# Optimization experiments

Hardware: AMD Instinct MI355X
Metric: run time of the kernel (lower is better)

Reference implementation:

```python
import jax, jax.numpy as jnp
import numpy as np

B, S, HID, NH, NKV, HD, PS = 4, 1024, 4096, 32, 8, 128, 16
PPS = S // PS            # pages per sequence
NP = B * PPS             # total pages
NNZ = B * S


def _llama31_freqs(head_dim):
    # flashinfer apply_llama31_rope defaults: theta=5e5, scale=8, low=1, high=4, old_ctx=8192
    half = head_dim // 2
    theta, scale, low_ff, high_ff, old_ctx = 500000.0, 8.0, 1.0, 4.0, 8192.0
    freq = 1.0 / (theta ** (jnp.arange(half, dtype=jnp.float32) * 2.0 / head_dim))
    wavelen = 2.0 * jnp.pi / freq
    low_wl, high_wl = old_ctx / low_ff, old_ctx / high_ff
    smooth = (old_ctx / wavelen - low_ff) / (high_ff - low_ff)
    return jnp.where(wavelen < high_wl, freq,
                     jnp.where(wavelen > low_wl, freq / scale,
                               (1.0 - smooth) * freq / scale + smooth * freq))


def _rope(x, pos, freqs):
    # x: [nnz, H, D], non-interleaved (rotate-half) layout
    ang = pos.astype(jnp.float32)[:, None] * freqs[None, :]          # [nnz, D/2]
    cos, sin = jnp.cos(ang)[:, None, :], jnp.sin(ang)[:, None, :]    # [nnz, 1, D/2]
    x1, x2 = jnp.split(x, 2, axis=-1)
    return jnp.concatenate([x1 * cos - x2 * sin, x2 * cos + x1 * sin], axis=-1)


def setup_inputs() -> dict:
    key = jax.random.key(0)
    ks = jax.random.split(key, 6)
    std = 0.02
    return {
        "hidden_states": jax.random.normal(ks[0], (NNZ, HID), jnp.float32),
        "wq": jax.random.normal(ks[1], (NH * HD, HID), jnp.float32) * std,
        "wk": jax.random.normal(ks[2], (NKV * HD, HID), jnp.float32) * std,
        "wv": jax.random.normal(ks[3], (NKV * HD, HID), jnp.float32) * std,
        "wo": jax.random.normal(ks[4], (HID, NH * HD), jnp.float32) * std,
        "kv_cache": jnp.zeros((1, NP, 2, PS, NKV, HD), jnp.float32),
        "position_ids": jnp.tile(jnp.arange(S, dtype=jnp.int32), B),
        "kv_page_indices": jnp.arange(NP, dtype=jnp.int32),
        "kv_page_indptr": jnp.arange(B + 1, dtype=jnp.int32) * PPS,
        "kv_last_page_lens": jnp.full((B,), PS, jnp.int32),
        "qo_indptr": jnp.arange(B + 1, dtype=jnp.int32) * S,
    }


def reference(hidden_states, wq, wk, wv, wo, kv_cache, position_ids,
              kv_page_indices, kv_page_indptr, kv_last_page_lens, qo_indptr):
    nnz = hidden_states.shape[0]
    b = qo_indptr.shape[0] - 1
    s = nnz // b
    # fused QKV projections (nn.Linear stores [out, in])
    q = (hidden_states @ wq.T).reshape(nnz, NH, HD)
    k = (hidden_states @ wk.T).reshape(nnz, NKV, HD)
    v = (hidden_states @ wv.T).reshape(nnz, NKV, HD)
    # inline Llama-3.1 RoPE with per-token position ids
    freqs = _llama31_freqs(HD)
    q = _rope(q, position_ids, freqs)
    k = _rope(k, position_ids, freqs)
    # paged-KV append: scatter k/v into pages at (page_id, slot)
    cache = kv_cache[0]                                   # [NP, 2, PS, NKV, HD]
    ps = cache.shape[2]
    pages = kv_page_indices.reshape(b, -1)                # [B, PPS]
    bidx = jnp.repeat(jnp.arange(b), s)
    pid = pages[bidx, position_ids // ps]
    slot = position_ids % ps
    cache = cache.at[pid, 0, slot].set(k).at[pid, 1, slot].set(v)
    # paged attention: gather per-sequence K/V from pages, causal SDPA with GQA
    flat = pages.reshape(-1)
    kf = cache[flat, 0].reshape(b, s, NKV, HD)
    vf = cache[flat, 1].reshape(b, s, NKV, HD)
    g = NH // NKV
    kr = jnp.repeat(kf, g, axis=2)                        # [B, S, NH, HD]
    vr = jnp.repeat(vf, g, axis=2)
    qb = q.reshape(b, s, NH, HD)
    scale = 1.0 / jnp.sqrt(jnp.float32(HD))
    scores = jnp.einsum('bqhd,bkhd->bhqk', qb, kr) * scale
    mask = jnp.tril(jnp.ones((s, s), bool))
    scores = jnp.where(mask[None, None], scores, jnp.float32(-1e30))
    attn = jax.nn.softmax(scores, axis=-1)
    out = jnp.einsum('bhqk,bkhd->bqhd', attn, vr).reshape(nnz, NH * HD)
    return out @ wo.T
```

## Files before the change

### kernel.cpp

```cpp
#include <hip/hip_runtime.h>

typedef unsigned short u16;
typedef __bf16 bf16x8 __attribute__((ext_vector_type(8)));
typedef float f32x4 __attribute__((ext_vector_type(4)));

__device__ __forceinline__ u16 f2bf(float f) {
  unsigned int u = __float_as_uint(f);
  u += 0x7fffu + ((u >> 16) & 1u);
  return (u16)(u >> 16);
}
__device__ __forceinline__ float bf2f(u16 v) {
  return __uint_as_float(((unsigned int)v) << 16);
}

__device__ __forceinline__ void gl_lds16(const u16* g, u16* l) {
  auto* lp = reinterpret_cast<__attribute__((address_space(3))) unsigned int*>(
      reinterpret_cast<uintptr_t>(l));
  auto* gp = reinterpret_cast<const __attribute__((address_space(1))) unsigned int*>(
      reinterpret_cast<uintptr_t>(g));
  __builtin_amdgcn_global_load_lds(gp, lp, 16, 0, 0);
}

__global__ __launch_bounds__(256) void cvt_kernel(const float* __restrict__ in,
                                                  u16* __restrict__ out, int n4) {
  int i = blockIdx.x * 256 + threadIdx.x;
  if (i >= n4) return;
  float4 v = ((const float4*)in)[i];
  ushort4 o;
  o.x = f2bf(v.x); o.y = f2bf(v.y); o.z = f2bf(v.z); o.w = f2bf(v.w);
  ((ushort4*)out)[i] = o;
}


#define BARRIER() __builtin_amdgcn_s_barrier()
#define VMCNT(n_) asm volatile("s_waitcnt vmcnt(" #n_ ")" ::: "memory")
#define PH_SYNC()                                           \
  do {                                                      \
    BARRIER();                                              \
    asm volatile("s_waitcnt lgkmcnt(0)" ::: "memory");      \
    __builtin_amdgcn_sched_barrier(0);                      \
  } while (0)

#define STAGE_A(b_, h_, kt_)                                                        \
  gl_lds16(gA + (size_t)((h_) * 128) * K + (size_t)(kt_) * 32,                      \
           lds + (b_) * 16384 + (h_) * 4096 + w * 512)

#define STAGE_B(b_, h_, kt_)                                                        \
  gl_lds16(gB + (size_t)((h_) * 128) * K + (size_t)(kt_) * 32,                      \
           lds + (b_) * 16384 + 8192 + (h_) * 4096 + w * 512)

#define LOADS_A(b_, qm_)                                                            \
  do {                                                                              \
    _Pragma("unroll") for (int i2 = 0; i2 < 4; i2++)                                \
      ar[i2] = *(const bf16x8*)&lds[(b_) * 16384 + arow + ((qm_)*4 + i2) * 512 + ax]; \
  } while (0)

#define LOADS_B(b_, qn_)                                                            \
  do {                                                                              \
    _Pragma("unroll") for (int j2 = 0; j2 < 2; j2++)                                \
      br[(qn_)*2 + j2] =                                                            \
          *(const bf16x8*)&lds[(b_) * 16384 + brow + ((qn_)*2 + j2) * 512 + ax];    \
  } while (0)

#define MFMA_Q(qm_, qn_)                                                            \
  do {                                                                              \
    __builtin_amdgcn_s_setprio(1);                                                  \
    _Pragma("unroll") for (int i2 = 0; i2 < 4; i2++) {                              \
      _Pragma("unroll") for (int j2 = 0; j2 < 2; j2++) {                            \
        acc[(qm_)*4 + i2][(qn_)*2 + j2] = __builtin_amdgcn_mfma_f32_16x16x32_bf16(  \
            ar[i2], br[(qn_)*2 + j2], acc[(qm_)*4 + i2][(qn_)*2 + j2], 0, 0, 0);    \
      }                                                                             \
    }                                                                               \
    __builtin_amdgcn_s_setprio(0);                                                  \
  } while (0)

template <int OUT_BF16>
__global__ __launch_bounds__(512, 2) void gemm8p(const u16* __restrict__ A,
                                                 const u16* __restrict__ B,
                                                 void* __restrict__ Cv,
                                                 int M, int N, int K) {
  __shared__ u16 lds[32768];
  (void)M;
  const int t = threadIdx.x, lane = t & 63, w = t >> 6;
  const int col = lane & 15, quad = lane >> 4;
  const int wm = w >> 2, wn = w & 3;

  const int nwg = gridDim.x * gridDim.y;
  const int wgid = blockIdx.y * gridDim.x + blockIdx.x;
  const int xcd = wgid & 7, lin = wgid >> 3;
  const int q8 = nwg >> 3, r8 = nwg & 7;
  const int nid = (xcd < r8 ? xcd * (q8 + 1) : r8 * (q8 + 1) + (xcd - r8) * q8) + lin;
  const int m0 = (nid / gridDim.x) * 256;
  const int n0 = (nid % gridDim.x) * 256;

  const int pr_ = t >> 3;
  const int s_ = (t & 7) ^ (pr_ & 7);
  const int srow = (pr_ << 1) | (s_ >> 2);
  const int sj = s_ & 3;
  const u16* gA = A + (size_t)(m0 + srow) * K + sj * 8;
  const u16* gB = B + (size_t)(n0 + srow) * K + sj * 8;

  const int arow = wm * 4096;
  const int brow = 8192 + wn * 2048;
  const int ax = (col >> 1) * 64 +
                 (((((col & 1) << 2) | quad) ^ (col >> 1)) << 3);

  f32x4 acc[8][4] = {};
  bf16x8 ar[4], br[4];

  STAGE_A(0, 0, 0); STAGE_A(0, 1, 0);
  STAGE_B(0, 0, 0); STAGE_B(0, 1, 0);
  STAGE_B(1, 0, 1); STAGE_B(1, 1, 1);
  VMCNT(2);
  BARRIER();

  const int NIT = K >> 6;
  for (int it = 0; it < NIT - 1; ++it) {
    const int kt = it * 2;
    LOADS_A(0, 0); LOADS_B(0, 0);
    STAGE_A(1, 0, kt + 1);
    PH_SYNC(); MFMA_Q(0, 0); BARRIER();
    LOADS_B(0, 1);
    STAGE_A(1, 1, kt + 1);
    PH_SYNC(); MFMA_Q(0, 1); BARRIER();
    LOADS_A(0, 1);
    STAGE_B(0, 0, kt + 2);
    PH_SYNC(); MFMA_Q(1, 0); BARRIER();
    STAGE_B(0, 1, kt + 2);
    PH_SYNC(); MFMA_Q(1, 1); VMCNT(2); BARRIER();
    LOADS_A(1, 0); LOADS_B(1, 0);
    STAGE_A(0, 0, kt + 2);
    PH_SYNC(); MFMA_Q(0, 0); BARRIER();
    LOADS_B(1, 1);
    STAGE_A(0, 1, kt + 2);
    PH_SYNC(); MFMA_Q(0, 1); BARRIER();
    LOADS_A(1, 1);
    STAGE_B(1, 0, kt + 3);
    PH_SYNC(); MFMA_Q(1, 0); BARRIER();
    STAGE_B(1, 1, kt + 3);
    PH_SYNC(); MFMA_Q(1, 1); VMCNT(2); BARRIER();
  }

  {
    const int kl = 2 * NIT - 1;
    LOADS_A(0, 0); LOADS_B(0, 0);
    STAGE_A(1, 0, kl);
    PH_SYNC(); MFMA_Q(0, 0); BARRIER();
    LOADS_B(0, 1);
    STAGE_A(1, 1, kl);
    PH_SYNC(); MFMA_Q(0, 1); BARRIER();
    LOADS_A(0, 1);
    PH_SYNC(); MFMA_Q(1, 0); BARRIER();
    PH_SYNC(); MFMA_Q(1, 1); VMCNT(0); BARRIER();
    LOADS_A(1, 0); LOADS_B(1, 0);
    PH_SYNC(); MFMA_Q(0, 0); BARRIER();
    LOADS_B(1, 1);
    PH_SYNC(); MFMA_Q(0, 1); BARRIER();
    LOADS_A(1, 1);
    PH_SYNC(); MFMA_Q(1, 0); BARRIER();
    MFMA_Q(1, 1);
  }

#pragma unroll
  for (int i = 0; i < 8; i++) {
#pragma unroll
    for (int j = 0; j < 4; j++) {
      const int mb = m0 + wm * 128 + i * 16 + quad * 4;
      const int n = n0 + wn * 64 + j * 16 + col;
#pragma unroll
      for (int r = 0; r < 4; r++) {
        float v = acc[i][j][r];
        if constexpr (OUT_BF16)
          ((u16*)Cv)[(size_t)(mb + r) * N + n] = f2bf(v);
        else
          ((float*)Cv)[(size_t)(mb + r) * N + n] = v;
      }
    }
  }
}

__global__ __launch_bounds__(256) void transpose_kernel(const u16* __restrict__ in,
                                                        u16* __restrict__ out,
                                                        int in_stride, int out_stride) {
  __shared__ u16 tile[64][72];
  const int t = threadIdx.x;
  const int bm = blockIdx.y;
  const int bn = blockIdx.x;
  const int r = t >> 3, c = (t & 7) * 8;
  const u16* src = in + (size_t)(bm * 64 + r) * in_stride + bn * 64 + c;
  *(uint4*)&tile[r][c] = *(const uint4*)src;
  *(uint4*)&tile[r + 32][c] = *(const uint4*)(src + (size_t)32 * in_stride);
  __syncthreads();
  u16 vals[8];
  u16* dst = out + (size_t)(bn * 64 + r) * out_stride + bm * 64 + c;
#pragma unroll
  for (int i = 0; i < 8; i++) vals[i] = tile[c + i][r];
  *(uint4*)dst = *(uint4*)vals;
#pragma unroll
  for (int i = 0; i < 8; i++) vals[i] = tile[c + i][r + 32];
  *(uint4*)(dst + (size_t)32 * out_stride) = *(uint4*)vals;
}

__global__ __launch_bounds__(256) void rope_kernel(u16* __restrict__ X,
                                                   const int* __restrict__ pos_ids,
                                                   int log2H, int row_stride) {
  int tid = blockIdx.x * 256 + threadIdx.x;
  int i = tid & 63;
  int rest = tid >> 6;
  int h = rest & ((1 << log2H) - 1);
  int token = rest >> log2H;
  float pos = (float)pos_ids[token];
  float fr = __builtin_exp2f(-(float)i * (18.93156856932417f / 64.0f));
  float wl = 6.283185307179586f / fr;
  float f2;
  if (wl < 2048.0f) f2 = fr;
  else if (wl > 8192.0f) f2 = fr * 0.125f;
  else {
    float sm = (8192.0f / wl - 1.0f) * (1.0f / 3.0f);
    f2 = (1.0f - sm) * fr * 0.125f + sm * fr;
  }
  float ang = pos * f2;
  float ss = sinf(ang), cc = cosf(ang);
  size_t base = (size_t)token * row_stride + (size_t)h * 128 + i;
  float x1 = bf2f(X[base]), x2 = bf2f(X[base + 64]);
  X[base] = f2bf(x1 * cc - x2 * ss);
  X[base + 64] = f2bf(x2 * cc + x1 * ss);
}

__global__ __launch_bounds__(256, 2) void attn_kernel(const u16* __restrict__ Qg,
                                                      const u16* __restrict__ Kg,
                                                      const u16* __restrict__ VTg,
                                                      u16* __restrict__ Og,
                                                      int QS, int KS) {
  const int qtp = 7 - blockIdx.x;
  const int qA = qtp * 2, qB = qA + 1;
  const int h = blockIdx.y, b = blockIdx.z;
  const int kvh = h >> 2;
  const int t = threadIdx.x, lane = t & 63, w = t >> 6;
  const int col = lane & 15, quad = lane >> 4;

  __shared__ u16 Ks[2][64 * 128];
  __shared__ u16 Vt[2][128 * 64];
  __shared__ u16 Ps[4][16][72];

  const u16* Kbase = Kg + (size_t)(b * 1024) * KS + kvh * 128;
  const u16* Vbase = VTg + (size_t)(kvh * 128) * 4096 + b * 1024;

  auto stage_kv = [&](int bb, int j) {
#pragma unroll
    for (int c = 0; c < 4; c++) {
      int ch = w * 4 + c;
      int krow = ch * 4 + (lane >> 4);
      int kg = (lane & 15) ^ (krow & 15);
      gl_lds16(Kbase + (size_t)(j * 64 + krow) * KS + kg * 8, &Ks[bb][ch * 512]);
      int vrow = ch * 8 + (lane >> 3);
      int vg = (lane & 7) ^ (vrow & 7);
      gl_lds16(Vbase + (size_t)vrow * 4096 + j * 64 + vg * 8, &Vt[bb][ch * 512]);
    }
  };

  {
    const u16* QbA = Qg + (size_t)(b * 1024 + qA * 64) * QS + h * 128;
    const u16* QbB = Qg + (size_t)(b * 1024 + qB * 64) * QS + h * 128;
#pragma unroll
    for (int c = 0; c < 4; c++) {
      int ch = w * 4 + c;
      int row = ch * 4 + (lane >> 4);
      int g = (lane & 15) ^ (row & 15);
      gl_lds16(QbA + (size_t)row * QS + g * 8, &Ks[0][ch * 512]);
      gl_lds16(QbB + (size_t)row * QS + g * 8, &Vt[0][ch * 512]);
    }
  }
  stage_kv(1, 0);
  __syncthreads();
  bf16x8 qaA[4], qaB[4];
#pragma unroll
  for (int kk = 0; kk < 4; kk++) {
    int row = w * 16 + col;
    int off = row * 128 + (((quad + 4 * kk) ^ col) << 3);
    qaA[kk] = *(const bf16x8*)&Ks[0][off];
    qaB[kk] = *(const bf16x8*)&Vt[0][off];
  }
  BARRIER();

  f32x4 oA[8] = {}, oB[8] = {};
  float mA[4] = {-3.0e38f, -3.0e38f, -3.0e38f, -3.0e38f};
  float mB[4] = {-3.0e38f, -3.0e38f, -3.0e38f, -3.0e38f};
  float lA[4] = {}, lB[4] = {};

  const float cf = 0.08838834764831845f * 1.4426950408889634f;
  const int qr0A = qA * 64 + w * 16 + quad * 4;
  const int qr0B = qB * 64 + w * 16 + quad * 4;

  auto process = [&](const u16* Ksb, const u16* Vtb, int j, bf16x8 (&qa)[4],
                     f32x4 (&o)[8], float (&m_i)[4], float (&l_i)[4], int qrow0) {
    f32x4 s[4] = {};
    __builtin_amdgcn_s_setprio(1);
#pragma unroll
    for (int nb = 0; nb < 4; nb++) {
      int key = nb * 16 + col;
#pragma unroll
      for (int kk = 0; kk < 4; kk++) {
        bf16x8 kb2 = *(const bf16x8*)&Ksb[key * 128 + (((quad + 4 * kk) ^ col) << 3)];
        s[nb] = __builtin_amdgcn_mfma_f32_16x16x32_bf16(qa[kk], kb2, s[nb], 0, 0, 0);
      }
    }
    __builtin_amdgcn_s_setprio(0);

#pragma unroll
    for (int nb = 0; nb < 4; nb++)
#pragma unroll
      for (int rr = 0; rr < 4; rr++)
        if (j * 64 + nb * 16 + col > qrow0 + rr) s[nb][rr] = -3.0e38f;

    float mnew[4];
#pragma unroll
    for (int rr = 0; rr < 4; rr++) {
      mnew[rr] = m_i[rr];
#pragma unroll
      for (int nb = 0; nb < 4; nb++) mnew[rr] = fmaxf(mnew[rr], s[nb][rr]);
    }
#pragma unroll
    for (int off = 1; off < 16; off <<= 1)
#pragma unroll
      for (int rr = 0; rr < 4; rr++)
        mnew[rr] = fmaxf(mnew[rr], __shfl_xor(mnew[rr], off));

    float p[4][4], rs[4], alpha[4];
#pragma unroll
    for (int rr = 0; rr < 4; rr++) {
      alpha[rr] = __builtin_exp2f((m_i[rr] - mnew[rr]) * cf);
      m_i[rr] = mnew[rr];
      rs[rr] = 0.0f;
    }
#pragma unroll
    for (int nb = 0; nb < 4; nb++)
#pragma unroll
      for (int rr = 0; rr < 4; rr++) {
        p[nb][rr] = __builtin_exp2f((s[nb][rr] - mnew[rr]) * cf);
        rs[rr] += p[nb][rr];
      }
#pragma unroll
    for (int off = 1; off < 16; off <<= 1)
#pragma unroll
      for (int rr = 0; rr < 4; rr++) rs[rr] += __shfl_xor(rs[rr], off);
#pragma unroll
    for (int rr = 0; rr < 4; rr++) l_i[rr] = l_i[rr] * alpha[rr] + rs[rr];
#pragma unroll
    for (int nb2 = 0; nb2 < 8; nb2++)
#pragma unroll
      for (int rr = 0; rr < 4; rr++) o[nb2][rr] *= alpha[rr];

#pragma unroll
    for (int nb = 0; nb < 4; nb++)
#pragma unroll
      for (int rr = 0; rr < 4; rr++)
        Ps[w][quad * 4 + rr][nb * 16 + col] = f2bf(p[nb][rr]);

    bf16x8 pa0 = *(const bf16x8*)&Ps[w][col][quad * 8];
    bf16x8 pa1 = *(const bf16x8*)&Ps[w][col][quad * 8 + 32];
    __builtin_amdgcn_s_setprio(1);
#pragma unroll
    for (int nb2 = 0; nb2 < 8; nb2++) {
      int d = nb2 * 16 + col;
      bf16x8 vb0 = *(const bf16x8*)&Vtb[d * 64 + ((quad ^ (col & 7)) << 3)];
      bf16x8 vb1 = *(const bf16x8*)&Vtb[d * 64 + ((((quad + 4) & 7) ^ (col & 7)) << 3)];
      o[nb2] = __builtin_amdgcn_mfma_f32_16x16x32_bf16(pa0, vb0, o[nb2], 0, 0, 0);
      o[nb2] = __builtin_amdgcn_mfma_f32_16x16x32_bf16(pa1, vb1, o[nb2], 0, 0, 0);
    }
    __builtin_amdgcn_s_setprio(0);
  };

  for (int j = 0; j <= qB; j++) {
    const int bb = (j + 1) & 1;
    if (j < qB) {
      stage_kv(bb ^ 1, j + 1);
      VMCNT(8);
    } else {
      VMCNT(0);
    }
    BARRIER();

    const u16* Ksb = &Ks[bb][0];
    const u16* Vtb = &Vt[bb][0];

    if (j <= qA) process(Ksb, Vtb, j, qaA, oA, mA, lA, qr0A);
    process(Ksb, Vtb, j, qaB, oB, mB, lB, qr0B);

    BARRIER();
  }

#pragma unroll
  for (int rr = 0; rr < 4; rr++) {
    float invA = 1.0f / lA[rr];
    float invB = 1.0f / lB[rr];
#pragma unroll
    for (int nb2 = 0; nb2 < 8; nb2++) {
      size_t offA = (size_t)(b * 1024 + qA * 64 + w * 16 + quad * 4 + rr) * 4096 +
                    h * 128 + nb2 * 16 + col;
      size_t offB = (size_t)(b * 1024 + qB * 64 + w * 16 + quad * 4 + rr) * 4096 +
                    h * 128 + nb2 * 16 + col;
      Og[offA] = f2bf(oA[nb2][rr] * invA);
      Og[offB] = f2bf(oB[nb2][rr] * invB);
    }
  }
}

extern "C" void kernel_launch(void* const* d_in, const int* in_sizes, int n_in,
                              void* d_out, int out_size, void* d_ws, size_t ws_size,
                              hipStream_t stream) {
  const float* hs = (const float*)d_in[0];
  const float* wq = (const float*)d_in[1];
  const float* wk = (const float*)d_in[2];
  const float* wv = (const float*)d_in[3];
  const float* wo = (const float*)d_in[4];
  const int* pos = (const int*)d_in[6];
  float* out = (float*)d_out;

  char* ws = (char*)d_ws;
  const size_t MB = 1ull << 20;
  u16* hs_bf   = (u16*)(ws + 0);
  u16* wqkv_bf = (u16*)(ws + 32 * MB);
  u16* QKV     = (u16*)(ws + 80 * MB);
  u16* wo_bf = (u16*)(ws + 0);
  u16* AOb   = (u16*)(ws + 32 * MB);
  u16* VTb   = (u16*)(ws + 64 * MB);

  cvt_kernel<<<16384, 256, 0, stream>>>(hs, hs_bf, 4194304);
  cvt_kernel<<<16384, 256, 0, stream>>>(wq, wqkv_bf, 4194304);
  cvt_kernel<<<4096, 256, 0, stream>>>(wk, wqkv_bf + 16777216, 1048576);
  cvt_kernel<<<4096, 256, 0, stream>>>(wv, wqkv_bf + 20971520, 1048576);

  gemm8p<1><<<dim3(24, 16), 512, 0, stream>>>(hs_bf, wqkv_bf, QKV, 4096, 6144, 4096);

  rope_kernel<<<32768, 256, 0, stream>>>(QKV, pos, 5, 6144);
  rope_kernel<<<8192, 256, 0, stream>>>(QKV + 4096, pos, 3, 6144);

  transpose_kernel<<<dim3(16, 64), 256, 0, stream>>>(QKV + 5120, VTb, 6144, 4096);

  cvt_kernel<<<16384, 256, 0, stream>>>(wo, wo_bf, 4194304);

  attn_kernel<<<dim3(8, 32, 4), 256, 0, stream>>>(QKV, QKV + 4096, VTb, AOb, 6144, 6144);

  gemm8p<0><<<dim3(16, 16), 512, 0, stream>>>(AOb, wo_bf, out, 4096, 4096, 4096);
}
```

Baseline: 784.6 us.

## Use 128x256-tile GEMM variant for output projection to double workgroup count

Adds a gemm4p kernel with 128x256 output tiles (half the M tile of gemm8p), a smaller LDS footprint and launch bounds allowing two workgroups per CU, and uses it for the final wo projection. The earlier grid of 256 workgroups on a 256-CU part gives one wave of large tiles. The new grid of 512 smaller tiles is meant to improve occupancy and latency hiding. The cost is lower arithmetic intensity per tile and more redundant B-tile loads.

```diff
diff --git a/kernel.cpp b/kernel.cpp
--- a/kernel.cpp
+++ b/kernel.cpp
@@ -31,7 +31,6 @@
   ((ushort4*)out)[i] = o;
 }
 
-
 #define BARRIER() __builtin_amdgcn_s_barrier()
 #define VMCNT(n_) asm volatile("s_waitcnt vmcnt(" #n_ ")" ::: "memory")
 #define PH_SYNC()                                           \
@@ -40,6 +39,7 @@
     asm volatile("s_waitcnt lgkmcnt(0)" ::: "memory");      \
     __builtin_amdgcn_sched_barrier(0);                      \
   } while (0)
+
 
 #define STAGE_A(b_, h_, kt_)                                                        \
   gl_lds16(gA + (size_t)((h_) * 128) * K + (size_t)(kt_) * 32,                      \
@@ -179,6 +179,126 @@
   }
 }
 
+
+#define G4_STAGE_A(b_, kt_)                                                         \
+  gl_lds16(gA + (size_t)(kt_) * 32, lds + (b_) * 12288 + w * 512)
+
+#define G4_STAGE_B(b_, h_, kt_)                                                     \
+  gl_lds16(gB + (size_t)((h_) * 128) * K + (size_t)(kt_) * 32,                      \
+           lds + (b_) * 12288 + 4096 + (h_) * 4096 + w * 512)
+
+#define G4_LOADS_B(b_)                                                              \
+  do {                                                                              \
+    _Pragma("unroll") for (int j2 = 0; j2 < 4; j2++)                                \
+      br[j2] = *(const bf16x8*)&lds[(b_) * 12288 + brow + j2 * 512 + ax];           \
+  } while (0)
+
+#define G4_LOADS_A(b_, h_)                                                          \
+  do {                                                                              \
+    _Pragma("unroll") for (int i2 = 0; i2 < 2; i2++)                                \
+      ar[(h_)*2 + i2] =                                                             \
+          *(const bf16x8*)&lds[(b_) * 12288 + arow + ((h_)*2 + i2) * 512 + ax];     \
+  } while (0)
+
+#define G4_MFMA(h_)                                                                 \
+  do {                                                                              \
+    __builtin_amdgcn_s_setprio(1);                                                  \
+    _Pragma("unroll") for (int i2 = 0; i2 < 2; i2++) {                              \
+      _Pragma("unroll") for (int j2 = 0; j2 < 4; j2++) {                            \
+        acc[(h_)*2 + i2][j2] = __builtin_amdgcn_mfma_f32_16x16x32_bf16(             \
+            ar[(h_)*2 + i2], br[j2], acc[(h_)*2 + i2][j2], 0, 0, 0);                \
+      }                                                                             \
+    }                                                                               \
+    __builtin_amdgcn_s_setprio(0);                                                  \
+  } while (0)
+
+template <int OUT_BF16>
+__global__ __launch_bounds__(512, 2) void gemm4p(const u16* __restrict__ A,
+                                                 const u16* __restrict__ B,
+                                                 void* __restrict__ Cv,
+                                                 int M, int N, int K) {
+  __shared__ u16 lds[24576];
+  (void)M;
+  const int t = threadIdx.x, lane = t & 63, w = t >> 6;
+  const int col = lane & 15, quad = lane >> 4;
+  const int wm = w >> 2, wn = w & 3;
+
+  const int nwg = gridDim.x * gridDim.y;
+  const int wgid = blockIdx.y * gridDim.x + blockIdx.x;
+  const int xcd = wgid & 7, lin = wgid >> 3;
+  const int q8 = nwg >> 3, r8 = nwg & 7;
+  const int nid = (xcd < r8 ? xcd * (q8 + 1) : r8 * (q8 + 1) + (xcd - r8) * q8) + lin;
+  const int m0 = (nid / gridDim.x) * 128;
+  const int n0 = (nid % gridDim.x) * 256;
+
+  const int pr_ = t >> 3;
+  const int s_ = (t & 7) ^ (pr_ & 7);
+  const int srow = (pr_ << 1) | (s_ >> 2);
+  const int sj = s_ & 3;
+  const u16* gA = A + (size_t)(m0 + srow) * K + sj * 8;
+  const u16* gB = B + (size_t)(n0 + srow) * K + sj * 8;
+
+  const int arow = wm * 2048;
+  const int brow = 4096 + wn * 2048;
+  const int ax = (col >> 1) * 64 +
+                 (((((col & 1) << 2) | quad) ^ (col >> 1)) << 3);
+
+  f32x4 acc[4][4] = {};
+  bf16x8 ar[4], br[4];
+
+  G4_STAGE_A(0, 0); G4_STAGE_B(0, 0, 0); G4_STAGE_B(0, 1, 0);
+  G4_STAGE_B(1, 0, 1); G4_STAGE_B(1, 1, 1);
+  VMCNT(2);
+  BARRIER();
+
+  const int NIT = K >> 6;
+  for (int it = 0; it < NIT - 1; ++it) {
+    const int kt = it * 2;
+    G4_LOADS_A(0, 0); G4_LOADS_B(0);
+    G4_STAGE_A(1, kt + 1);
+    PH_SYNC(); G4_MFMA(0); BARRIER();
+    G4_LOADS_A(0, 1);
+    G4_STAGE_B(0, 0, kt + 2); G4_STAGE_B(0, 1, kt + 2);
+    PH_SYNC(); G4_MFMA(1); VMCNT(2); BARRIER();
+    G4_LOADS_A(1, 0); G4_LOADS_B(1);
+    G4_STAGE_A(0, kt + 2);
+    PH_SYNC(); G4_MFMA(0); BARRIER();
+    G4_LOADS_A(1, 1);
+    G4_STAGE_B(1, 0, kt + 3); G4_STAGE_B(1, 1, kt + 3);
+    PH_SYNC(); G4_MFMA(1); VMCNT(2); BARRIER();
+  }
+
+  {
+    const int kl = 2 * NIT - 1;
+    G4_LOADS_A(0, 0); G4_LOADS_B(0);
+    G4_STAGE_A(1, kl);
+    PH_SYNC(); G4_MFMA(0); BARRIER();
+    G4_LOADS_A(0, 1);
+    PH_SYNC(); G4_MFMA(1); VMCNT(0); BARRIER();
+    G4_LOADS_A(1, 0); G4_LOADS_B(1);
+    PH_SYNC(); G4_MFMA(0); BARRIER();
+    G4_LOADS_A(1, 1);
+    PH_SYNC(); G4_MFMA(1);
+  }
+
+#pragma unroll
+  for (int i = 0; i < 4; i++) {
+#pragma unroll
+    for (int j = 0; j < 4; j++) {
+      const int mb = m0 + wm * 64 + i * 16 + quad * 4;
+      const int n = n0 + wn * 64 + j * 16 + col;
+#pragma unroll
+      for (int r = 0; r < 4; r++) {
+        float v = acc[i][j][r];
+        if constexpr (OUT_BF16)
+          ((u16*)Cv)[(size_t)(mb + r) * N + n] = f2bf(v);
+        else
+          ((float*)Cv)[(size_t)(mb + r) * N + n] = v;
+      }
+    }
+  }
+}
+
 __global__ __launch_bounds__(256) void transpose_kernel(const u16* __restrict__ in,
                                                         u16* __restrict__ out,
                                                         int in_stride, int out_stride) {
@@ -442,5 +562,5 @@
 
   attn_kernel<<<dim3(8, 32, 4), 256, 0, stream>>>(QKV, QKV + 4096, VTb, AOb, 6144, 6144);
 
-  gemm8p<0><<<dim3(16, 16), 512, 0, stream>>>(AOb, wo_bf, out, 4096, 4096, 4096);
-}
+  gemm4p<0><<<dim3(16, 32), 512, 0, stream>>>(AOb, wo_bf, out, 4096, 4096, 4096);
+}
```

Result: slower. 824.9 us (+5.1%).
